# Kernel tuning notes

Measured on AMD Instinct MI355X. Metric: run time of the kernel, lower is better.

## Reference

```python
import jax, jax.numpy as jnp
from jax import lax
import numpy as np

B, C, FH, FW, H, V, L = 256, 512, 8, 16, 512, 64, 24


def setup_inputs() -> dict:
    key = jax.random.key(0)
    ks = jax.random.split(key, 32)
    s = 0.05
    n = lambda k, shp: jax.random.normal(k, shp, dtype=jnp.float32) * s
    return {
        "encoder_ftrs": jax.random.normal(ks[0], (B, C, FH, FW), dtype=jnp.float32),
        "sequences": jax.random.randint(ks[1], (B, L), 0, V),
        "test": 0,
        "embed_w": n(ks[2], (V, H)),
        "init_state": n(ks[3], (2, 1, H)),
        "attn_W_w": n(ks[4], (H, C)), "attn_W_b": jnp.zeros((H,), jnp.float32),
        "attn_U_w": n(ks[5], (H, H)), "attn_U_b": jnp.zeros((H,), jnp.float32),
        "attn_v_w": n(ks[6], (1, H)), "attn_v_b": jnp.zeros((1,), jnp.float32),
        "fc_w": n(ks[7], (H, C + H)), "fc_b": jnp.zeros((H,), jnp.float32),
        "cls_w": n(ks[8], (V, H)), "cls_b": jnp.zeros((V,), jnp.float32),
        "gru0_wih": n(ks[9], (3 * H, 2 * H)), "gru0_whh": n(ks[10], (3 * H, H)),
        "gru0_bih": jnp.zeros((3 * H,), jnp.float32), "gru0_bhh": jnp.zeros((3 * H,), jnp.float32),
        "gru1_wih": n(ks[11], (3 * H, H)), "gru1_whh": n(ks[12], (3 * H, H)),
        "gru1_bih": jnp.zeros((3 * H,), jnp.float32), "gru1_bhh": jnp.zeros((3 * H,), jnp.float32),
    }


def _gru_cell(x, h, wih, whh, bih, bhh):
    # PyTorch GRUCell: r,z gates then candidate n with r applied on hidden path
    gi = x @ wih.T + bih
    gh = h @ whh.T + bhh
    i_r, i_z, i_n = jnp.split(gi, 3, axis=-1)
    h_r, h_z, h_n = jnp.split(gh, 3, axis=-1)
    r = jax.nn.sigmoid(i_r + h_r)
    z = jax.nn.sigmoid(i_z + h_z)
    nact = jnp.tanh(i_n + r * h_n)
    return (1.0 - z) * nact + z * h


def reference(encoder_ftrs, sequences, test, embed_w, init_state,
              attn_W_w, attn_W_b, attn_U_w, attn_U_b, attn_v_w, attn_v_b,
              fc_w, fc_b, cls_w, cls_b,
              gru0_wih, gru0_whh, gru0_bih, gru0_bhh,
              gru1_wih, gru1_whh, gru1_bih, gru1_bhh):
    bsz = encoder_ftrs.shape[0]
    # [B, L_sp, C] encoder states
    states = encoder_ftrs.reshape(bsz, C, -1).transpose(0, 2, 1)
    # attn_W(states) is timestep-independent: precompute once (same math)
    Ws = states @ attn_W_w.T + attn_W_b  # [B, L_sp, H]

    def apply_attn(h_top):
        e = jax.nn.relu(Ws + (h_top @ attn_U_w.T + attn_U_b)[:, None, :])
        scores = e @ attn_v_w[0] + attn_v_b[0]          # [B, L_sp]
        a = jax.nn.softmax(scores, axis=-1)
        ctx = jnp.einsum('bl,blc->bc', a, states)        # [B, C]
        return ctx

    def out_proj(ctx, h_top):
        return jax.nn.relu(jnp.concatenate([ctx, h_top], axis=-1) @ fc_w.T + fc_b)

    xs = embed_w[sequences[:, :-1]]                      # [B, T, H]
    h0 = jnp.broadcast_to(init_state, (2, bsz, H))       # repeat over batch
    y0 = out_proj(apply_attn(h0[1]), h0[1])              # time_step == -1 (output dropped)

    def step(carry, x_t):
        h, y = carry
        h_l0 = _gru_cell(jnp.concatenate([y, x_t], axis=-1), h[0],
                         gru0_wih, gru0_whh, gru0_bih, gru0_bhh)
        h_l1 = _gru_cell(h_l0, h[1], gru1_wih, gru1_whh, gru1_bih, gru1_bhh)
        hn = jnp.stack([h_l0, h_l1], axis=0)
        yn = out_proj(apply_attn(h_l1), h_l1)
        return (hn, yn), yn

    _, ys = lax.scan(step, (h0, y0), xs.transpose(1, 0, 2))   # [T, B, H]
    logits = ys.transpose(1, 0, 2) @ cls_w.T + cls_b          # [B, T, V]

    labels = sequences[:, 1:]
    mask = (labels > 0).astype(logits.dtype)
    logp = jax.nn.log_softmax(logits, axis=-1)
    nll = -jnp.take_along_axis(logp, labels[..., None], axis=-1)[..., 0]
    loss = jnp.sum(nll * mask) / jnp.sum(mask)
    return loss
```

## Files before the change

kernel.cpp:

```cpp
#include <hip/hip_runtime.h>
#include <hip/hip_bf16.h>
#include <cstddef>

#define BB 256
#define CC 512
#define SS 128
#define HH 512
#define VV 64
#define LL 24

typedef unsigned short ush;
typedef __attribute__((ext_vector_type(8))) short short8;
typedef __attribute__((ext_vector_type(4))) float f32x4;

__device__ __forceinline__ float wave_sum(float v) {
#pragma unroll
    for (int off = 32; off > 0; off >>= 1) v += __shfl_xor(v, off);
    return v;
}
__device__ __forceinline__ float wave_max(float v) {
#pragma unroll
    for (int off = 32; off > 0; off >>= 1) v = fmaxf(v, __shfl_xor(v, off));
    return v;
}
__device__ __forceinline__ float sigm(float x) { return 1.0f / (1.0f + expf(-x)); }
__device__ __forceinline__ ush f2bf(float f) {
    unsigned u = __float_as_uint(f);
    u += 0x7FFFu + ((u >> 16) & 1u);
    return (ush)(u >> 16);
}
__device__ __forceinline__ float bf2f(ush b) {
    return __uint_as_float(((unsigned)b) << 16);
}
__device__ __forceinline__ unsigned pack2(float a, float b) {
    return (unsigned)f2bf(a) | ((unsigned)f2bf(b) << 16);
}

__global__ __launch_bounds__(256) void init_kernel(const float* __restrict__ init_state,
                                                   float* __restrict__ h0,
                                                   float* __restrict__ h1,
                                                   ush* __restrict__ h0b,
                                                   ush* __restrict__ h1b,
                                                   float* __restrict__ acc) {
    int idx = blockIdx.x * 256 + threadIdx.x;
    if (idx < BB * HH) {
        float a = init_state[idx & (HH - 1)];
        float b = init_state[HH + (idx & (HH - 1))];
        h0[idx] = a; h1[idx] = b;
        h0b[idx] = f2bf(a); h1b[idx] = f2bf(b);
    }
    if (idx < 2) acc[idx] = 0.0f;
}

__global__ __launch_bounds__(256) void conv_kernel(const float* __restrict__ src,
                                                   ush* __restrict__ dst, int n4) {
    int i = blockIdx.x * 256 + threadIdx.x;
    if (i < n4) {
        float4 v = ((const float4*)src)[i];
        uint2 o;
        o.x = pack2(v.x, v.y);
        o.y = pack2(v.z, v.w);
        ((uint2*)dst)[i] = o;
    }
}

__global__ __launch_bounds__(128) void gather_kernel(const float* __restrict__ embed_w,
                                                     const int* __restrict__ seq,
                                                     ush* __restrict__ xall) {
    int item = blockIdx.x;
    int t = item >> 8, m = item & 255;
    int row = seq[m * LL + t];
    float4 v = ((const float4*)(embed_w + (size_t)row * HH))[threadIdx.x];
    uint2 o;
    o.x = pack2(v.x, v.y);
    o.y = pack2(v.z, v.w);
    ((uint2*)(xall + (size_t)item * HH))[threadIdx.x] = o;
}

__global__ __launch_bounds__(256) void enc_conv(const float* __restrict__ enc,
                                                ush* __restrict__ enc_t) {
    int b = blockIdx.x, cg = blockIdx.y;
    int c0 = cg * 128;
    __shared__ ush tile[128][130];
    const float* src = enc + ((size_t)b * 512 + c0) * 128;
#pragma unroll
    for (int i = 0; i < 16; i++) {
        int lin = i * 256 + threadIdx.x;
        int cl = lin >> 5, s4 = lin & 31;
        float4 v = ((const float4*)(src + (size_t)cl * 128))[s4];
        ush b0 = f2bf(v.x), b1 = f2bf(v.y), b2 = f2bf(v.z), b3 = f2bf(v.w);
        tile[s4 * 4 + 0][cl] = b0;
        tile[s4 * 4 + 1][cl] = b1;
        tile[s4 * 4 + 2][cl] = b2;
        tile[s4 * 4 + 3][cl] = b3;
    }
    __syncthreads();
#pragma unroll
    for (int i = 0; i < 16; i++) {
        int lin = i * 256 + threadIdx.x;
        int sl = lin >> 5, c4 = lin & 31;
        ush a0 = tile[sl][c4 * 4 + 0], a1 = tile[sl][c4 * 4 + 1];
        ush a2 = tile[sl][c4 * 4 + 2], a3 = tile[sl][c4 * 4 + 3];
        uint2 o;
        o.x = (unsigned)a0 | ((unsigned)a1 << 16);
        o.y = (unsigned)a2 | ((unsigned)a3 << 16);
        ((uint2*)(enc_t + ((size_t)b * 128 + sl) * 512 + c0))[c4] = o;
    }
}

__global__ __launch_bounds__(256) void ws_v2(const ush* __restrict__ enc_t,
                                             const ush* __restrict__ Wb,
                                             const float* __restrict__ bias,
                                             ush* __restrict__ Ws_bf) {
    int tid = threadIdx.x;
    int wave = tid >> 6, lane = tid & 63;
    int quad = lane >> 4, l16 = lane & 15;
    int m0 = blockIdx.x * 128 + wave * 32;
    int n0 = blockIdx.y * 128;
    const ush* ap = enc_t + (size_t)(m0 + l16) * 512 + quad * 8;
    const ush* bp = Wb + (size_t)(n0 + l16) * 512 + quad * 8;
    f32x4 acc[2][8];
#pragma unroll
    for (int f = 0; f < 2; f++)
#pragma unroll
        for (int s = 0; s < 8; s++) acc[f][s] = (f32x4){0.f, 0.f, 0.f, 0.f};
    short8 ac[2], bc[8], an[2], bn[8];
    ac[0] = *(const short8*)(ap);
    ac[1] = *(const short8*)(ap + (size_t)16 * 512);
#pragma unroll
    for (int s = 0; s < 8; s++) bc[s] = *(const short8*)(bp + (size_t)s * 16 * 512);
#pragma unroll
    for (int ks = 0; ks < 16; ks++) {
        if (ks < 15) {
            int k = (ks + 1) * 32;
            an[0] = *(const short8*)(ap + k);
            an[1] = *(const short8*)(ap + (size_t)16 * 512 + k);
#pragma unroll
            for (int s = 0; s < 8; s++)
                bn[s] = *(const short8*)(bp + (size_t)s * 16 * 512 + k);
        }
#pragma unroll
        for (int f = 0; f < 2; f++)
#pragma unroll
            for (int s = 0; s < 8; s++)
                acc[f][s] = __builtin_amdgcn_mfma_f32_16x16x32_bf16(ac[f], bc[s], acc[f][s], 0, 0, 0);
        if (ks < 15) {
            ac[0] = an[0]; ac[1] = an[1];
#pragma unroll
            for (int s = 0; s < 8; s++) bc[s] = bn[s];
        }
    }
#pragma unroll
    for (int s = 0; s < 8; s++) {
        int n = n0 + s * 16 + l16;
        float bs = bias[n];
#pragma unroll
        for (int f = 0; f < 2; f++)
#pragma unroll
            for (int r = 0; r < 4; r++) {
                int m = m0 + f * 16 + quad * 4 + r;
                Ws_bf[(size_t)m * HH + n] = f2bf(acc[f][s][r] + bs);
            }
    }
}

template <int NSTEP>
__device__ __forceinline__ void segk(const ush* __restrict__ ap,
                                     const ush* __restrict__ bp,
                                     size_t wofs, f32x4& a0, f32x4& a1) {
    short8 as[4], bs0[4], bs1[4];
    constexpr int PRE = NSTEP < 4 ? NSTEP : 4;
#pragma unroll
    for (int i = 0; i < PRE; i++) {
        as[i]  = *(const short8*)(ap + 32 * i);
        bs0[i] = *(const short8*)(bp + 32 * i);
        bs1[i] = *(const short8*)(bp + wofs + 32 * i);
    }
#pragma unroll
    for (int i = 0; i < NSTEP; i++) {
        const int sl = i & 3;
        a0 = __builtin_amdgcn_mfma_f32_16x16x32_bf16(as[sl], bs0[sl], a0, 0, 0, 0);
        a1 = __builtin_amdgcn_mfma_f32_16x16x32_bf16(as[sl], bs1[sl], a1, 0, 0, 0);
        if (i + 4 < NSTEP) {
            as[sl]  = *(const short8*)(ap + 32 * (i + 4));
            bs0[sl] = *(const short8*)(bp + 32 * (i + 4));
            bs1[sl] = *(const short8*)(bp + wofs + 32 * (i + 4));
        }
    }
}

struct GruArgs {
    const ush* xs[8][2];
    const ush* wb[8][2];
    int wst[8][2];
    int nks[8][2];
    int slot[8][2];
    int zmask;
};

__global__ __launch_bounds__(512) void gru_fused(GruArgs A,
                                                 const float* __restrict__ h_prev,
                                                 const float* __restrict__ bih,
                                                 const float* __restrict__ bhh,
                                                 float* __restrict__ h_out,
                                                 ush* __restrict__ h_out_bf) {
    int tid = threadIdx.x;
    int wave = __builtin_amdgcn_readfirstlane(tid >> 6);
    int lane = tid & 63, quad = lane >> 4, l16 = lane & 15;
    int m0 = blockIdx.x * 16, n0 = blockIdx.y * 32;
    __shared__ float gbuf[10][16][32];
    if (A.zmask) {
        int mi = tid >> 5, ni = tid & 31;
#pragma unroll
        for (int s = 0; s < 10; s++)
            if ((A.zmask >> s) & 1) gbuf[s][mi][ni] = 0.0f;
    }
    for (int e = 0; e < 2; e++) {
        int nks = A.nks[wave][e];
        if (nks == 0) continue;
        f32x4 a0 = (f32x4){0.f, 0.f, 0.f, 0.f};
        f32x4 a1 = (f32x4){0.f, 0.f, 0.f, 0.f};
        int wst = A.wst[wave][e];
        const ush* ap = A.xs[wave][e] + (size_t)(m0 + l16) * 512 + quad * 8;
        const ush* bp = A.wb[wave][e] + (size_t)(n0 + l16) * wst + quad * 8;
        size_t wofs = (size_t)16 * wst;
        if (nks == 16) segk<16>(ap, bp, wofs, a0, a1);
        else           segk<8>(ap, bp, wofs, a0, a1);
        int sl = A.slot[wave][e];
#pragma unroll
        for (int r = 0; r < 4; r++) {
            gbuf[sl][quad * 4 + r][l16]      = a0[r];
            gbuf[sl][quad * 4 + r][16 + l16] = a1[r];
        }
    }
    __syncthreads();
    {
        int mi = tid >> 5, ni = tid & 31;
        int n = n0 + ni;
        size_t off = (size_t)(m0 + mi) * HH + n;
        float r  = sigm(gbuf[0][mi][ni] + gbuf[1][mi][ni] + gbuf[2][mi][ni] +
                        bih[n] + bhh[n]);
        float zf = sigm(gbuf[3][mi][ni] + gbuf[4][mi][ni] + gbuf[5][mi][ni] +
                        bih[512 + n] + bhh[512 + n]);
        float na = tanhf(gbuf[6][mi][ni] + gbuf[7][mi][ni] + bih[1024 + n] +
                         r * (gbuf[8][mi][ni] + gbuf[9][mi][ni] + bhh[1024 + n]));
        float hp = h_prev[off];
        float ho = (1.0f - zf) * na + zf * hp;
        h_out[off] = ho;
        h_out_bf[off] = f2bf(ho);
    }
}

__global__ __launch_bounds__(512) void fc_fused(const ush* __restrict__ ctx,
                                                const ush* __restrict__ h,
                                                const ush* __restrict__ wFc,
                                                const float* __restrict__ bias,
                                                ush* __restrict__ y,
                                                ush* __restrict__ ys) {
    int tid = threadIdx.x;
    int wave = __builtin_amdgcn_readfirstlane(tid >> 6);
    int lane = tid & 63, quad = lane >> 4, l16 = lane & 15;
    int m0 = blockIdx.x * 16, n0 = blockIdx.y * 32;
    const ush* X = (wave < 4) ? ctx : h;
    int q = wave & 3;
    f32x4 a0 = (f32x4){0.f, 0.f, 0.f, 0.f};
    f32x4 a1 = (f32x4){0.f, 0.f, 0.f, 0.f};
    const ush* ap = X + (size_t)(m0 + l16) * 512 + q * 128 + quad * 8;
    const ush* bp = wFc + (size_t)(n0 + l16) * 1024 + (wave >= 4 ? 512 : 0) + q * 128 + quad * 8;
    segk<4>(ap, bp, (size_t)16 * 1024, a0, a1);
    __shared__ float gbuf[8][16][32];
#pragma unroll
    for (int r = 0; r < 4; r++) {
        gbuf[wave][quad * 4 + r][l16]      = a0[r];
        gbuf[wave][quad * 4 + r][16 + l16] = a1[r];
    }
    __syncthreads();
    {
        int mi = tid >> 5, ni = tid & 31;
        int n = n0 + ni;
        float v = bias[n];
#pragma unroll
        for (int w = 0; w < 8; w++) v += gbuf[w][mi][ni];
        v = fmaxf(v, 0.0f);
        ush bb = f2bf(v);
        size_t off = (size_t)(m0 + mi) * HH + n;
        y[off] = bb;
        if (ys) ys[off] = bb;
    }
}

__global__ __launch_bounds__(512) void u_fused(const ush* __restrict__ h,
                                               const ush* __restrict__ wU,
                                               const float* __restrict__ Ub,
                                               float* __restrict__ Uo) {
    int tid = threadIdx.x;
    int wave = __builtin_amdgcn_readfirstlane(tid >> 6);
    int lane = tid & 63, quad = lane >> 4, l16 = lane & 15;
    int m0 = blockIdx.x * 16, n0 = blockIdx.y * 32;
    f32x4 a0 = (f32x4){0.f, 0.f, 0.f, 0.f};
    f32x4 a1 = (f32x4){0.f, 0.f, 0.f, 0.f};
    const ush* ap = h + (size_t)(m0 + l16) * 512 + wave * 64 + quad * 8;
    const ush* bp = wU + (size_t)(n0 + l16) * 512 + wave * 64 + quad * 8;
    segk<2>(ap, bp, (size_t)16 * 512, a0, a1);
    __shared__ float gbuf[8][16][32];
#pragma unroll
    for (int r = 0; r < 4; r++) {
        gbuf[wave][quad * 4 + r][l16]      = a0[r];
        gbuf[wave][quad * 4 + r][16 + l16] = a1[r];
    }
    __syncthreads();
    {
        int mi = tid >> 5, ni = tid & 31;
        int n = n0 + ni;
        float v = Ub[n];
#pragma unroll
        for (int w = 0; w < 8; w++) v += gbuf[w][mi][ni];
        Uo[(size_t)(m0 + mi) * HH + n] = v;
    }
}

__global__ __launch_bounds__(512) void attn3(const float* __restrict__ u,
                                             const float* __restrict__ vw,
                                             const ush* __restrict__ Ws_bf,
                                             const ush* __restrict__ enc_t,
                                             ush* __restrict__ ctx_bf) {
    int b = blockIdx.x;
    int tid = threadIdx.x;
    int wave = tid >> 6, lane = tid & 63;
    int hi = lane >> 4, li = lane & 15;
    __shared__ float a[SS];
    __shared__ float part[8][512];

    float ur[4][8], vr[4][8];
#pragma unroll
    for (int p = 0; p < 4; p++) {
        const float* up = u + (size_t)b * HH + p * 128 + li * 8;
        const float* vp = vw + p * 128 + li * 8;
        float4 u0 = *(const float4*)(up);
        float4 u1 = *(const float4*)(up + 4);
        float4 v0 = *(const float4*)(vp);
        float4 v1 = *(const float4*)(vp + 4);
        ur[p][0] = u0.x; ur[p][1] = u0.y; ur[p][2] = u0.z; ur[p][3] = u0.w;
        ur[p][4] = u1.x; ur[p][5] = u1.y; ur[p][6] = u1.z; ur[p][7] = u1.w;
        vr[p][0] = v0.x; vr[p][1] = v0.y; vr[p][2] = v0.z; vr[p][3] = v0.w;
        vr[p][4] = v1.x; vr[p][5] = v1.y; vr[p][6] = v1.z; vr[p][7] = v1.w;
    }
    const ush* wsb = Ws_bf + (size_t)b * SS * HH;
#pragma unroll
    for (int pass = 0; pass < 4; pass++) {
        int s = pass * 32 + wave * 4 + hi;
        float acc = 0.0f;
#pragma unroll
        for (int p = 0; p < 4; p++) {
            short8 rv = *(const short8*)(wsb + (size_t)s * HH + p * 128 + li * 8);
#pragma unroll
            for (int j = 0; j < 8; j++) {
                float e = bf2f((ush)rv[j]) + ur[p][j];
                acc += fmaxf(e, 0.0f) * vr[p][j];
            }
        }
#pragma unroll
        for (int off = 1; off < 16; off <<= 1) acc += __shfl_xor(acc, off);
        if (li == 0) a[s] = acc;
    }
    __syncthreads();
    if (wave == 0) {
        float s0v = a[lane], s1v = a[lane + 64];
        float m = wave_max(fmaxf(s0v, s1v));
        float e0 = expf(s0v - m), e1 = expf(s1v - m);
        float ssum = wave_sum(e0 + e1);
        float inv = 1.0f / ssum;
        a[lane] = e0 * inv;
        a[lane + 64] = e1 * inv;
    }
    __syncthreads();
    float c8[8];
#pragma unroll
    for (int j = 0; j < 8; j++) c8[j] = 0.0f;
    const ush* ebt = enc_t + (size_t)b * SS * 512;
#pragma unroll
    for (int i = 0; i < 16; i++) {
        int s = wave * 16 + i;
        float as = a[s];
        short8 ev = *(const short8*)(ebt + (size_t)s * 512 + lane * 8);
#pragma unroll
        for (int j = 0; j < 8; j++) c8[j] += as * bf2f((ush)ev[j]);
    }
    *(float4*)(&part[wave][lane * 8])     = (float4){c8[0], c8[1], c8[2], c8[3]};
    *(float4*)(&part[wave][lane * 8 + 4]) = (float4){c8[4], c8[5], c8[6], c8[7]};
    __syncthreads();
    {
        float sum = 0.0f;
#pragma unroll
        for (int w = 0; w < 8; w++) sum += part[w][tid];
        ctx_bf[(size_t)b * CC + tid] = f2bf(sum);
    }
}

__global__ __launch_bounds__(256) void cls_fused(const ush* __restrict__ ys,
                                                 const ush* __restrict__ wCls,
                                                 const float* __restrict__ cls_b,
                                                 const int* __restrict__ seq,
                                                 float* __restrict__ acc) {
    int tid = threadIdx.x;
    int wave = tid >> 6, lane = tid & 63;
    int quad = lane >> 4, l16 = lane & 15;
    int m0 = blockIdx.x * 16;
    f32x4 a4[4];
#pragma unroll
    for (int s = 0; s < 4; s++) a4[s] = (f32x4){0.f, 0.f, 0.f, 0.f};
    const ush* ap = ys + (size_t)(m0 + l16) * 512 + wave * 128 + quad * 8;
    const ush* bp = wCls + (size_t)l16 * 512 + wave * 128 + quad * 8;
#pragma unroll
    for (int ks = 0; ks < 4; ks++) {
        short8 av = *(const short8*)(ap + ks * 32);
#pragma unroll
        for (int s = 0; s < 4; s++) {
            short8 bv = *(const short8*)(bp + (size_t)s * 16 * 512 + ks * 32);
            a4[s] = __builtin_amdgcn_mfma_f32_16x16x32_bf16(av, bv, a4[s], 0, 0, 0);
        }
    }
    __shared__ float gbuf[4][16][64];
    __shared__ float red[8];
#pragma unroll
    for (int s = 0; s < 4; s++)
#pragma unroll
        for (int r = 0; r < 4; r++)
            gbuf[wave][quad * 4 + r][s * 16 + l16] = a4[s][r];
    __syncthreads();
    float lsum = 0.0f, lcnt = 0.0f;
#pragma unroll
    for (int ii = 0; ii < 4; ii++) {
        int mi = wave * 4 + ii;
        int item = m0 + mi;
        int t = item >> 8, b = item & 255;
        float v = gbuf[0][mi][lane] + gbuf[1][mi][lane] + gbuf[2][mi][lane] +
                  gbuf[3][mi][lane] + cls_b[lane];
        float mx = wave_max(v);
        float e = expf(v - mx);
        float ssum = wave_sum(e);
        int label = seq[b * LL + t + 1];
        float vl = __shfl(v, label);
        if (label > 0) {
            lsum += -(vl - mx - logf(ssum));
            lcnt += 1.0f;
        }
    }
    if (lane == 0) { red[wave] = lsum; red[4 + wave] = lcnt; }
    __syncthreads();
    if (tid == 0) {
        atomicAdd(&acc[0], red[0] + red[1] + red[2] + red[3]);
        atomicAdd(&acc[1], red[4] + red[5] + red[6] + red[7]);
    }
}

__global__ void final_kernel(const float* __restrict__ acc, float* __restrict__ out) {
    if (threadIdx.x == 0) out[0] = acc[0] / acc[1];
}

extern "C" void kernel_launch(void* const* d_in, const int* in_sizes, int n_in,
                              void* d_out, int out_size, void* d_ws, size_t ws_size,
                              hipStream_t stream) {
    const float* enc        = (const float*)d_in[0];
    const int*   seq        = (const int*)d_in[1];
    const float* embed_w    = (const float*)d_in[3];
    const float* init_state = (const float*)d_in[4];
    const float* attn_W_w   = (const float*)d_in[5];
    const float* attn_W_b   = (const float*)d_in[6];
    const float* attn_U_w   = (const float*)d_in[7];
    const float* attn_U_b   = (const float*)d_in[8];
    const float* attn_v_w   = (const float*)d_in[9];
    const float* fc_w       = (const float*)d_in[11];
    const float* fc_b       = (const float*)d_in[12];
    const float* cls_w      = (const float*)d_in[13];
    const float* cls_b      = (const float*)d_in[14];
    const float* g0_wih     = (const float*)d_in[15];
    const float* g0_whh     = (const float*)d_in[16];
    const float* g0_bih     = (const float*)d_in[17];
    const float* g0_bhh     = (const float*)d_in[18];
    const float* g1_wih     = (const float*)d_in[19];
    const float* g1_whh     = (const float*)d_in[20];
    const float* g1_bih     = (const float*)d_in[21];
    const float* g1_bhh     = (const float*)d_in[22];
    float* out = (float*)d_out;

    float* ws = (float*)d_ws;
    size_t o = 0;
    ush* Ws_bf   = (ush*)(ws + o); o += (size_t)BB * SS * HH / 2;
    ush* enc_t   = (ush*)(ws + o); o += (size_t)BB * CC * SS / 2;
    ush* ys_bf   = (ush*)(ws + o); o += (size_t)(LL - 1) * BB * HH / 2;
    ush* xall_bf = (ush*)(ws + o); o += (size_t)(LL - 1) * BB * HH / 2;
    ush* wWb  = (ush*)(ws + o); o += 262144 / 2;
    ush* wU   = (ush*)(ws + o); o += 262144 / 2;
    ush* wFc  = (ush*)(ws + o); o += 524288 / 2;
    ush* wCls = (ush*)(ws + o); o += 32768 / 2;
    ush* wG0i = (ush*)(ws + o); o += 1572864 / 2;
    ush* wG0h = (ush*)(ws + o); o += 786432 / 2;
    ush* wG1i = (ush*)(ws + o); o += 786432 / 2;
    ush* wG1h = (ush*)(ws + o); o += 786432 / 2;
    float* Uo   = ws + o; o += (size_t)BB * HH;
    float* h0a  = ws + o; o += (size_t)BB * HH;
    float* h0b  = ws + o; o += (size_t)BB * HH;
    float* h1a  = ws + o; o += (size_t)BB * HH;
    float* h1b  = ws + o; o += (size_t)BB * HH;
    float* acc  = ws + o; o += 256;
    ush* h0a_bf = (ush*)(ws + o); o += (size_t)BB * HH / 2;
    ush* h0b_bf = (ush*)(ws + o); o += (size_t)BB * HH / 2;
    ush* h1a_bf = (ush*)(ws + o); o += (size_t)BB * HH / 2;
    ush* h1b_bf = (ush*)(ws + o); o += (size_t)BB * HH / 2;
    ush* y_bf   = (ush*)(ws + o); o += (size_t)BB * HH / 2;
    ush* ctx_bf = (ush*)(ws + o); o += (size_t)BB * CC / 2;

    init_kernel<<<512, 256, 0, stream>>>(init_state, h0a, h1a, h0a_bf, h1a_bf, acc);
    conv_kernel<<<256, 256, 0, stream>>>(attn_W_w, wWb, 65536);
    conv_kernel<<<256, 256, 0, stream>>>(attn_U_w, wU, 65536);
    conv_kernel<<<512, 256, 0, stream>>>(fc_w, wFc, 131072);
    conv_kernel<<<32, 256, 0, stream>>>(cls_w, wCls, 8192);
    conv_kernel<<<1536, 256, 0, stream>>>(g0_wih, wG0i, 393216);
    conv_kernel<<<768, 256, 0, stream>>>(g0_whh, wG0h, 196608);
    conv_kernel<<<768, 256, 0, stream>>>(g1_wih, wG1i, 196608);
    conv_kernel<<<768, 256, 0, stream>>>(g1_whh, wG1h, 196608);
    enc_conv<<<dim3(256, 4), 256, 0, stream>>>(enc, enc_t);
    gather_kernel<<<(LL - 1) * BB, 128, 0, stream>>>(embed_w, seq, xall_bf);
    ws_v2<<<dim3(256, 4), 256, 0, stream>>>(enc_t, wWb, attn_W_b, Ws_bf);

    auto setw = [](GruArgs& a, int w, int e, const ush* xs, const ush* wb,
                   int wst, int nks, int slot) {
        a.xs[w][e] = xs; a.wb[w][e] = wb; a.wst[w][e] = wst;
        a.nks[w][e] = nks; a.slot[w][e] = slot;
    };
    auto gru0_args = [&](const ush* y, const ush* x, const ush* h0) {
        GruArgs a{};
        setw(a, 0, 0, y,        wG0i,                             1024, 16, 0);
        setw(a, 1, 0, x,        wG0i + 512,                       1024, 16, 1);
        setw(a, 2, 0, h0,       wG0h,                              512, 16, 2);
        setw(a, 3, 0, y,        wG0i + (size_t)512 * 1024,        1024, 16, 3);
        setw(a, 4, 0, x,        wG0i + (size_t)512 * 1024 + 512,  1024, 16, 4);
        setw(a, 5, 0, h0,       wG0h + (size_t)512 * 512,          512, 16, 5);
        setw(a, 6, 0, y,        wG0i + (size_t)1024 * 1024,       1024, 16, 6);
        setw(a, 7, 0, x,        wG0i + (size_t)1024 * 1024 + 512, 1024, 16, 7);
        setw(a, 6, 1, h0,       wG0h + (size_t)1024 * 512,         512,  8, 8);
        setw(a, 7, 1, h0 + 256, wG0h + (size_t)1024 * 512 + 256,   512,  8, 9);
        a.zmask = 0;
        return a;
    };
    auto gru1_args = [&](const ush* hl0, const ush* h1) {
        GruArgs a{};
        setw(a, 0, 0, hl0,       wG1i,                             512, 16, 0);
        setw(a, 1, 0, h1,        wG1h,                             512, 16, 1);
        setw(a, 2, 0, hl0,       wG1i + (size_t)512 * 512,         512, 16, 3);
        setw(a, 3, 0, h1,        wG1h + (size_t)512 * 512,         512, 16, 4);
        setw(a, 4, 0, hl0,       wG1i + (size_t)1024 * 512,        512,  8, 6);
        setw(a, 5, 0, hl0 + 256, wG1i + (size_t)1024 * 512 + 256,  512,  8, 7);
        setw(a, 6, 0, h1,        wG1h + (size_t)1024 * 512,        512,  8, 8);
        setw(a, 7, 0, h1 + 256,  wG1h + (size_t)1024 * 512 + 256,  512,  8, 9);
        a.zmask = (1 << 2) | (1 << 5);
        return a;
    };

    u_fused<<<dim3(16, 16), 512, 0, stream>>>(h1a_bf, wU, attn_U_b, Uo);
    attn3<<<BB, 512, 0, stream>>>(Uo, attn_v_w, Ws_bf, enc_t, ctx_bf);
    fc_fused<<<dim3(16, 16), 512, 0, stream>>>(ctx_bf, h1a_bf, wFc, fc_b, y_bf, nullptr);

    float* h0_in = h0a; float* h0_out = h0b;
    float* h1_in = h1a; float* h1_out = h1b;
    ush* h0_in_bf = h0a_bf; ush* h0_out_bf = h0b_bf;
    ush* h1_in_bf = h1a_bf; ush* h1_out_bf = h1b_bf;
    for (int t = 0; t < LL - 1; t++) {
        gru_fused<<<dim3(16, 16), 512, 0, stream>>>(
            gru0_args(y_bf, xall_bf + (size_t)t * BB * HH, h0_in_bf),
            h0_in, g0_bih, g0_bhh, h0_out, h0_out_bf);
        gru_fused<<<dim3(16, 16), 512, 0, stream>>>(
            gru1_args(h0_out_bf, h1_in_bf),
            h1_in, g1_bih, g1_bhh, h1_out, h1_out_bf);
        u_fused<<<dim3(16, 16), 512, 0, stream>>>(h1_out_bf, wU, attn_U_b, Uo);
        attn3<<<BB, 512, 0, stream>>>(Uo, attn_v_w, Ws_bf, enc_t, ctx_bf);
        fc_fused<<<dim3(16, 16), 512, 0, stream>>>(ctx_bf, h1_out_bf, wFc, fc_b,
                                                   y_bf, ys_bf + (size_t)t * BB * HH);
        float* tmp;
        tmp = h0_in; h0_in = h0_out; h0_out = tmp;
        tmp = h1_in; h1_in = h1_out; h1_out = tmp;
        ush* tb;
        tb = h0_in_bf; h0_in_bf = h0_out_bf; h0_out_bf = tb;
        tb = h1_in_bf; h1_in_bf = h1_out_bf; h1_out_bf = tb;
    }

    cls_fused<<<368, 256, 0, stream>>>(ys_bf, wCls, cls_b, seq, acc);
    final_kernel<<<1, 1, 0, stream>>>(acc, out);
}
```

Baseline: 1.395 ms.

## Fuse U-projection, attention and fc into one per-batch kernel; retile GRU and prep

```diff
diff --git a/kernel.cpp b/kernel.cpp
--- a/kernel.cpp
+++ b/kernel.cpp
@@ -32,6 +32,8 @@
 __device__ __forceinline__ float bf2f(ush b) {
     return __uint_as_float(((unsigned)b) << 16);
 }
+__device__ __forceinline__ float bfl(unsigned u) { return __uint_as_float(u << 16); }
+__device__ __forceinline__ float bfh(unsigned u) { return __uint_as_float(u & 0xFFFF0000u); }
 __device__ __forceinline__ unsigned pack2(float a, float b) {
     return (unsigned)f2bf(a) | ((unsigned)f2bf(b) << 16);
 }
@@ -52,15 +54,50 @@
     if (idx < 2) acc[idx] = 0.0f;
 }
 
-__global__ __launch_bounds__(256) void conv_kernel(const float* __restrict__ src,
-                                                   ush* __restrict__ dst, int n4) {
-    int i = blockIdx.x * 256 + threadIdx.x;
-    if (i < n4) {
-        float4 v = ((const float4*)src)[i];
+struct CvArgs {
+    const float* src[6];
+    ush* dst[6];
+    int end[6];
+};
+__global__ __launch_bounds__(256) void conv_multi(CvArgs A) {
+    int blk = blockIdx.x;
+    int s = 0;
+    while (s < 5 && blk >= A.end[s]) s++;
+    int base = s ? A.end[s - 1] : 0;
+    int i = (blk - base) * 256 + threadIdx.x;
+    float4 v = ((const float4*)A.src[s])[i];
+    uint2 o;
+    o.x = pack2(v.x, v.y);
+    o.y = pack2(v.z, v.w);
+    ((uint2*)A.dst[s])[i] = o;
+}
+
+__global__ __launch_bounds__(256) void tp_conv(const float* __restrict__ src,
+                                               uint2* __restrict__ dst, int K) {
+    int n0 = blockIdx.x * 64, k0 = blockIdx.y * 64;
+    __shared__ ush til[64][68];
+    int tid = threadIdx.x;
+#pragma unroll
+    for (int i = 0; i < 4; i++) {
+        int idx = i * 256 + tid;
+        int r = idx >> 4, c4 = idx & 15;
+        float4 v = ((const float4*)(src + (size_t)(n0 + r) * K + k0))[c4];
+        til[r][c4 * 4 + 0] = f2bf(v.x);
+        til[r][c4 * 4 + 1] = f2bf(v.y);
+        til[r][c4 * 4 + 2] = f2bf(v.z);
+        til[r][c4 * 4 + 3] = f2bf(v.w);
+    }
+    __syncthreads();
+#pragma unroll
+    for (int i = 0; i < 4; i++) {
+        int idx = i * 256 + tid;
+        int k4l = idx >> 6, nl = idx & 63;
+        ush t0 = til[nl][k4l * 4 + 0], t1 = til[nl][k4l * 4 + 1];
+        ush t2 = til[nl][k4l * 4 + 2], t3 = til[nl][k4l * 4 + 3];
         uint2 o;
-        o.x = pack2(v.x, v.y);
-        o.y = pack2(v.z, v.w);
-        ((uint2*)dst)[i] = o;
+        o.x = (unsigned)t0 | ((unsigned)t1 << 16);
+        o.y = (unsigned)t2 | ((unsigned)t3 << 16);
+        dst[(size_t)(k0 / 4 + k4l) * 512 + n0 + nl] = o;
     }
 }
 
@@ -88,11 +125,10 @@
         int lin = i * 256 + threadIdx.x;
         int cl = lin >> 5, s4 = lin & 31;
         float4 v = ((const float4*)(src + (size_t)cl * 128))[s4];
-        ush b0 = f2bf(v.x), b1 = f2bf(v.y), b2 = f2bf(v.z), b3 = f2bf(v.w);
-        tile[s4 * 4 + 0][cl] = b0;
-        tile[s4 * 4 + 1][cl] = b1;
-        tile[s4 * 4 + 2][cl] = b2;
-        tile[s4 * 4 + 3][cl] = b3;
+        tile[s4 * 4 + 0][cl] = f2bf(v.x);
+        tile[s4 * 4 + 1][cl] = f2bf(v.y);
+        tile[s4 * 4 + 2][cl] = f2bf(v.z);
+        tile[s4 * 4 + 3][cl] = f2bf(v.w);
     }
     __syncthreads();
 #pragma unroll
@@ -108,54 +144,56 @@
     }
 }
 
-__global__ __launch_bounds__(256) void ws_v2(const ush* __restrict__ enc_t,
+__global__ __launch_bounds__(512) void ws_v3(const ush* __restrict__ enc_t,
                                              const ush* __restrict__ Wb,
                                              const float* __restrict__ bias,
                                              ush* __restrict__ Ws_bf) {
     int tid = threadIdx.x;
     int wave = tid >> 6, lane = tid & 63;
     int quad = lane >> 4, l16 = lane & 15;
-    int m0 = blockIdx.x * 128 + wave * 32;
-    int n0 = blockIdx.y * 128;
+    int m0 = blockIdx.x * 128 + (wave & 1) * 64;
+    int n0 = blockIdx.y * 128 + (wave >> 1) * 32;
     const ush* ap = enc_t + (size_t)(m0 + l16) * 512 + quad * 8;
     const ush* bp = Wb + (size_t)(n0 + l16) * 512 + quad * 8;
-    f32x4 acc[2][8];
-#pragma unroll
-    for (int f = 0; f < 2; f++)
-#pragma unroll
-        for (int s = 0; s < 8; s++) acc[f][s] = (f32x4){0.f, 0.f, 0.f, 0.f};
-    short8 ac[2], bc[8], an[2], bn[8];
-    ac[0] = *(const short8*)(ap);
-    ac[1] = *(const short8*)(ap + (size_t)16 * 512);
-#pragma unroll
-    for (int s = 0; s < 8; s++) bc[s] = *(const short8*)(bp + (size_t)s * 16 * 512);
+    f32x4 acc[4][2];
+#pragma unroll
+    for (int f = 0; f < 4; f++)
+#pragma unroll
+        for (int s = 0; s < 2; s++) acc[f][s] = (f32x4){0.f, 0.f, 0.f, 0.f};
+    short8 ac[4], bc[2], an[4], bn[2];
+#pragma unroll
+    for (int f = 0; f < 4; f++) ac[f] = *(const short8*)(ap + (size_t)f * 16 * 512);
+#pragma unroll
+    for (int s = 0; s < 2; s++) bc[s] = *(const short8*)(bp + (size_t)s * 16 * 512);
 #pragma unroll
     for (int ks = 0; ks < 16; ks++) {
         if (ks < 15) {
             int k = (ks + 1) * 32;
-            an[0] = *(const short8*)(ap + k);
-            an[1] = *(const short8*)(ap + (size_t)16 * 512 + k);
-#pragma unroll
-            for (int s = 0; s < 8; s++)
+#pragma unroll
+            for (int f = 0; f < 4; f++)
+                an[f] = *(const short8*)(ap + (size_t)f * 16 * 512 + k);
+#pragma unroll
+            for (int s = 0; s < 2; s++)
                 bn[s] = *(const short8*)(bp + (size_t)s * 16 * 512 + k);
         }
 #pragma unroll
-        for (int f = 0; f < 2; f++)
-#pragma unroll
-            for (int s = 0; s < 8; s++)
+        for (int f = 0; f < 4; f++)
+#pragma unroll
+            for (int s = 0; s < 2; s++)
                 acc[f][s] = __builtin_amdgcn_mfma_f32_16x16x32_bf16(ac[f], bc[s], acc[f][s], 0, 0, 0);
         if (ks < 15) {
-            ac[0] = an[0]; ac[1] = an[1];
-#pragma unroll
-            for (int s = 0; s < 8; s++) bc[s] = bn[s];
-        }
-    }
-#pragma unroll
-    for (int s = 0; s < 8; s++) {
+#pragma unroll
+            for (int f = 0; f < 4; f++) ac[f] = an[f];
+#pragma unroll
+            for (int s = 0; s < 2; s++) bc[s] = bn[s];
+        }
+    }
+#pragma unroll
+    for (int s = 0; s < 2; s++) {
         int n = n0 + s * 16 + l16;
         float bs = bias[n];
 #pragma unroll
-        for (int f = 0; f < 2; f++)
+        for (int f = 0; f < 4; f++)
 #pragma unroll
             for (int r = 0; r < 4; r++) {
                 int m = m0 + f * 16 + quad * 4 + r;
@@ -165,38 +203,28 @@
 }
 
 template <int NSTEP>
-__device__ __forceinline__ void segk(const ush* __restrict__ ap,
-                                     const ush* __restrict__ bp,
-                                     size_t wofs, f32x4& a0, f32x4& a1) {
-    short8 as[4], bs0[4], bs1[4];
+__device__ __forceinline__ void segk1(const ush* __restrict__ ap,
+                                      const ush* __restrict__ bp, f32x4& a0) {
+    short8 as[4], bs[4];
     constexpr int PRE = NSTEP < 4 ? NSTEP : 4;
 #pragma unroll
     for (int i = 0; i < PRE; i++) {
-        as[i]  = *(const short8*)(ap + 32 * i);
-        bs0[i] = *(const short8*)(bp + 32 * i);
-        bs1[i] = *(const short8*)(bp + wofs + 32 * i);
+        as[i] = *(const short8*)(ap + 32 * i);
+        bs[i] = *(const short8*)(bp + 32 * i);
     }
 #pragma unroll
     for (int i = 0; i < NSTEP; i++) {
         const int sl = i & 3;
-        a0 = __builtin_amdgcn_mfma_f32_16x16x32_bf16(as[sl], bs0[sl], a0, 0, 0, 0);
-        a1 = __builtin_amdgcn_mfma_f32_16x16x32_bf16(as[sl], bs1[sl], a1, 0, 0, 0);
+        a0 = __builtin_amdgcn_mfma_f32_16x16x32_bf16(as[sl], bs[sl], a0, 0, 0, 0);
         if (i + 4 < NSTEP) {
-            as[sl]  = *(const short8*)(ap + 32 * (i + 4));
-            bs0[sl] = *(const short8*)(bp + 32 * (i + 4));
-            bs1[sl] = *(const short8*)(bp + wofs + 32 * (i + 4));
-        }
-    }
-}
-
-struct GruArgs {
-    const ush* xs[8][2];
-    const ush* wb[8][2];
-    int wst[8][2];
-    int nks[8][2];
-    int slot[8][2];
-    int zmask;
-};
+            as[sl] = *(const short8*)(ap + 32 * (i + 4));
+            bs[sl] = *(const short8*)(bp + 32 * (i + 4));
+        }
+    }
+}
+
+struct GruEnt { const ush* x; const ush* w; int wst; int nks; int slot; };
+struct GruArgs { GruEnt e[8][2]; int zmask; };
 
 __global__ __launch_bounds__(512) void gru_fused(GruArgs A,
                                                  const float* __restrict__ h_prev,
@@ -207,43 +235,41 @@
     int tid = threadIdx.x;
     int wave = __builtin_amdgcn_readfirstlane(tid >> 6);
     int lane = tid & 63, quad = lane >> 4, l16 = lane & 15;
-    int m0 = blockIdx.x * 16, n0 = blockIdx.y * 32;
-    __shared__ float gbuf[10][16][32];
-    if (A.zmask) {
-        int mi = tid >> 5, ni = tid & 31;
-#pragma unroll
-        for (int s = 0; s < 10; s++)
+    int m0 = blockIdx.x * 16, n0 = blockIdx.y * 16;
+    __shared__ float gbuf[14][16][16];
+    if (tid < 256 && A.zmask) {
+        int mi = tid >> 4, ni = tid & 15;
+#pragma unroll
+        for (int s = 0; s < 14; s++)
             if ((A.zmask >> s) & 1) gbuf[s][mi][ni] = 0.0f;
     }
+#pragma unroll
     for (int e = 0; e < 2; e++) {
-        int nks = A.nks[wave][e];
-        if (nks == 0) continue;
+        GruEnt ent = A.e[wave][e];
+        if (ent.nks == 0) continue;
         f32x4 a0 = (f32x4){0.f, 0.f, 0.f, 0.f};
-        f32x4 a1 = (f32x4){0.f, 0.f, 0.f, 0.f};
-        int wst = A.wst[wave][e];
-        const ush* ap = A.xs[wave][e] + (size_t)(m0 + l16) * 512 + quad * 8;
-        const ush* bp = A.wb[wave][e] + (size_t)(n0 + l16) * wst + quad * 8;
-        size_t wofs = (size_t)16 * wst;
-        if (nks == 16) segk<16>(ap, bp, wofs, a0, a1);
-        else           segk<8>(ap, bp, wofs, a0, a1);
-        int sl = A.slot[wave][e];
-#pragma unroll
-        for (int r = 0; r < 4; r++) {
-            gbuf[sl][quad * 4 + r][l16]      = a0[r];
-            gbuf[sl][quad * 4 + r][16 + l16] = a1[r];
-        }
-    }
-    __syncthreads();
-    {
-        int mi = tid >> 5, ni = tid & 31;
+        const ush* ap = ent.x + (size_t)(m0 + l16) * 512 + quad * 8;
+        const ush* bp = ent.w + (size_t)(n0 + l16) * ent.wst + quad * 8;
+        if (ent.nks == 16)      segk1<16>(ap, bp, a0);
+        else if (ent.nks == 12) segk1<12>(ap, bp, a0);
+        else if (ent.nks == 8)  segk1<8>(ap, bp, a0);
+        else                    segk1<4>(ap, bp, a0);
+#pragma unroll
+        for (int r = 0; r < 4; r++)
+            gbuf[ent.slot][quad * 4 + r][l16] = a0[r];
+    }
+    __syncthreads();
+    if (tid < 256) {
+        int mi = tid >> 4, ni = tid & 15;
         int n = n0 + ni;
         size_t off = (size_t)(m0 + mi) * HH + n;
-        float r  = sigm(gbuf[0][mi][ni] + gbuf[1][mi][ni] + gbuf[2][mi][ni] +
-                        bih[n] + bhh[n]);
-        float zf = sigm(gbuf[3][mi][ni] + gbuf[4][mi][ni] + gbuf[5][mi][ni] +
-                        bih[512 + n] + bhh[512 + n]);
-        float na = tanhf(gbuf[6][mi][ni] + gbuf[7][mi][ni] + bih[1024 + n] +
-                         r * (gbuf[8][mi][ni] + gbuf[9][mi][ni] + bhh[1024 + n]));
+        float rr = sigm(gbuf[0][mi][ni] + gbuf[1][mi][ni] + gbuf[2][mi][ni] +
+                        gbuf[3][mi][ni] + bih[n] + bhh[n]);
+        float zf = sigm(gbuf[4][mi][ni] + gbuf[5][mi][ni] + gbuf[6][mi][ni] +
+                        gbuf[7][mi][ni] + bih[512 + n] + bhh[512 + n]);
+        float na = tanhf(gbuf[8][mi][ni] + gbuf[9][mi][ni] + bih[1024 + n] +
+                         rr * (gbuf[10][mi][ni] + gbuf[11][mi][ni] +
+                               gbuf[12][mi][ni] + gbuf[13][mi][ni] + bhh[1024 + n]));
         float hp = h_prev[off];
         float ho = (1.0f - zf) * na + zf * hp;
         h_out[off] = ho;
@@ -251,93 +277,49 @@
     }
 }
 
-__global__ __launch_bounds__(512) void fc_fused(const ush* __restrict__ ctx,
-                                                const ush* __restrict__ h,
-                                                const ush* __restrict__ wFc,
-                                                const float* __restrict__ bias,
-                                                ush* __restrict__ y,
-                                                ush* __restrict__ ys) {
-    int tid = threadIdx.x;
-    int wave = __builtin_amdgcn_readfirstlane(tid >> 6);
-    int lane = tid & 63, quad = lane >> 4, l16 = lane & 15;
-    int m0 = blockIdx.x * 16, n0 = blockIdx.y * 32;
-    const ush* X = (wave < 4) ? ctx : h;
-    int q = wave & 3;
-    f32x4 a0 = (f32x4){0.f, 0.f, 0.f, 0.f};
-    f32x4 a1 = (f32x4){0.f, 0.f, 0.f, 0.f};
-    const ush* ap = X + (size_t)(m0 + l16) * 512 + q * 128 + quad * 8;
-    const ush* bp = wFc + (size_t)(n0 + l16) * 1024 + (wave >= 4 ? 512 : 0) + q * 128 + quad * 8;
-    segk<4>(ap, bp, (size_t)16 * 1024, a0, a1);
-    __shared__ float gbuf[8][16][32];
-#pragma unroll
-    for (int r = 0; r < 4; r++) {
-        gbuf[wave][quad * 4 + r][l16]      = a0[r];
-        gbuf[wave][quad * 4 + r][16 + l16] = a1[r];
-    }
-    __syncthreads();
-    {
-        int mi = tid >> 5, ni = tid & 31;
-        int n = n0 + ni;
-        float v = bias[n];
-#pragma unroll
-        for (int w = 0; w < 8; w++) v += gbuf[w][mi][ni];
-        v = fmaxf(v, 0.0f);
-        ush bb = f2bf(v);
-        size_t off = (size_t)(m0 + mi) * HH + n;
-        y[off] = bb;
-        if (ys) ys[off] = bb;
-    }
-}
-
-__global__ __launch_bounds__(512) void u_fused(const ush* __restrict__ h,
-                                               const ush* __restrict__ wU,
-                                               const float* __restrict__ Ub,
-                                               float* __restrict__ Uo) {
-    int tid = threadIdx.x;
-    int wave = __builtin_amdgcn_readfirstlane(tid >> 6);
-    int lane = tid & 63, quad = lane >> 4, l16 = lane & 15;
-    int m0 = blockIdx.x * 16, n0 = blockIdx.y * 32;
-    f32x4 a0 = (f32x4){0.f, 0.f, 0.f, 0.f};
-    f32x4 a1 = (f32x4){0.f, 0.f, 0.f, 0.f};
-    const ush* ap = h + (size_t)(m0 + l16) * 512 + wave * 64 + quad * 8;
-    const ush* bp = wU + (size_t)(n0 + l16) * 512 + wave * 64 + quad * 8;
-    segk<2>(ap, bp, (size_t)16 * 512, a0, a1);
-    __shared__ float gbuf[8][16][32];
-#pragma unroll
-    for (int r = 0; r < 4; r++) {
-        gbuf[wave][quad * 4 + r][l16]      = a0[r];
-        gbuf[wave][quad * 4 + r][16 + l16] = a1[r];
-    }
-    __syncthreads();
-    {
-        int mi = tid >> 5, ni = tid & 31;
-        int n = n0 + ni;
-        float v = Ub[n];
-#pragma unroll
-        for (int w = 0; w < 8; w++) v += gbuf[w][mi][ni];
-        Uo[(size_t)(m0 + mi) * HH + n] = v;
-    }
-}
-
-__global__ __launch_bounds__(512) void attn3(const float* __restrict__ u,
-                                             const float* __restrict__ vw,
-                                             const ush* __restrict__ Ws_bf,
-                                             const ush* __restrict__ enc_t,
-                                             ush* __restrict__ ctx_bf) {
+__global__ __launch_bounds__(512) void uaf(const float* __restrict__ h1f,
+                                           const uint2* __restrict__ wUt,
+                                           const float* __restrict__ Ub,
+                                           const float* __restrict__ vw,
+                                           const ush* __restrict__ Ws_bf,
+                                           const ush* __restrict__ enc_t,
+                                           const uint2* __restrict__ wFcT,
+                                           const float* __restrict__ fc_b,
+                                           ush* __restrict__ y_bf,
+                                           ush* __restrict__ ys_bf) {
     int b = blockIdx.x;
     int tid = threadIdx.x;
     int wave = tid >> 6, lane = tid & 63;
     int hi = lane >> 4, li = lane & 15;
+    __shared__ float h1s[512];
+    __shared__ float u_lds[512];
+    __shared__ float ctx[512];
     __shared__ float a[SS];
     __shared__ float part[8][512];
 
+    h1s[tid] = h1f[(size_t)b * HH + tid];
+    __syncthreads();
+
+    {
+        float acc = Ub[tid];
+        const uint2* wp = wUt + tid;
+#pragma unroll 8
+        for (int kq = 0; kq < 128; kq++) {
+            uint2 pr = wp[(size_t)kq * 512];
+            float x0 = h1s[kq * 4 + 0], x1 = h1s[kq * 4 + 1];
+            float x2 = h1s[kq * 4 + 2], x3 = h1s[kq * 4 + 3];
+            acc += bfl(pr.x) * x0 + bfh(pr.x) * x1 + bfl(pr.y) * x2 + bfh(pr.y) * x3;
+        }
+        u_lds[tid] = acc;
+    }
+    __syncthreads();
+
     float ur[4][8], vr[4][8];
 #pragma unroll
     for (int p = 0; p < 4; p++) {
-        const float* up = u + (size_t)b * HH + p * 128 + li * 8;
+        float4 u0 = *(const float4*)(&u_lds[p * 128 + li * 8]);
+        float4 u1 = *(const float4*)(&u_lds[p * 128 + li * 8 + 4]);
         const float* vp = vw + p * 128 + li * 8;
-        float4 u0 = *(const float4*)(up);
-        float4 u1 = *(const float4*)(up + 4);
         float4 v0 = *(const float4*)(vp);
         float4 v1 = *(const float4*)(vp + 4);
         ur[p][0] = u0.x; ur[p][1] = u0.y; ur[p][2] = u0.z; ur[p][3] = u0.w;
@@ -364,6 +346,7 @@
         if (li == 0) a[s] = acc;
     }
     __syncthreads();
+
     if (wave == 0) {
         float s0v = a[lane], s1v = a[lane + 64];
         float m = wave_max(fmaxf(s0v, s1v));
@@ -374,26 +357,54 @@
         a[lane + 64] = e1 * inv;
     }
     __syncthreads();
-    float c8[8];
-#pragma unroll
-    for (int j = 0; j < 8; j++) c8[j] = 0.0f;
-    const ush* ebt = enc_t + (size_t)b * SS * 512;
-#pragma unroll
-    for (int i = 0; i < 16; i++) {
-        int s = wave * 16 + i;
-        float as = a[s];
-        short8 ev = *(const short8*)(ebt + (size_t)s * 512 + lane * 8);
-#pragma unroll
-        for (int j = 0; j < 8; j++) c8[j] += as * bf2f((ush)ev[j]);
-    }
-    *(float4*)(&part[wave][lane * 8])     = (float4){c8[0], c8[1], c8[2], c8[3]};
-    *(float4*)(&part[wave][lane * 8 + 4]) = (float4){c8[4], c8[5], c8[6], c8[7]};
+
+    {
+        float c8[8];
+#pragma unroll
+        for (int j = 0; j < 8; j++) c8[j] = 0.0f;
+        const ush* ebt = enc_t + (size_t)b * SS * 512;
+#pragma unroll
+        for (int i = 0; i < 16; i++) {
+            int s = wave * 16 + i;
+            float as = a[s];
+            short8 ev = *(const short8*)(ebt + (size_t)s * 512 + lane * 8);
+#pragma unroll
+            for (int j = 0; j < 8; j++) c8[j] += as * bf2f((ush)ev[j]);
+        }
+        *(float4*)(&part[wave][lane * 8])     = (float4){c8[0], c8[1], c8[2], c8[3]};
+        *(float4*)(&part[wave][lane * 8 + 4]) = (float4){c8[4], c8[5], c8[6], c8[7]};
+    }
     __syncthreads();
     {
         float sum = 0.0f;
 #pragma unroll
         for (int w = 0; w < 8; w++) sum += part[w][tid];
-        ctx_bf[(size_t)b * CC + tid] = f2bf(sum);
+        ctx[tid] = sum;
+    }
+    __syncthreads();
+
+    {
+        float acc = fc_b[tid];
+        const uint2* wp = wFcT + tid;
+#pragma unroll 8
+        for (int kq = 0; kq < 128; kq++) {
+            uint2 pr = wp[(size_t)kq * 512];
+            float x0 = ctx[kq * 4 + 0], x1 = ctx[kq * 4 + 1];
+            float x2 = ctx[kq * 4 + 2], x3 = ctx[kq * 4 + 3];
+            acc += bfl(pr.x) * x0 + bfh(pr.x) * x1 + bfl(pr.y) * x2 + bfh(pr.y) * x3;
+        }
+#pragma unroll 8
+        for (int kq = 128; kq < 256; kq++) {
+            uint2 pr = wp[(size_t)kq * 512];
+            int k = kq * 4 - 512;
+            float x0 = h1s[k + 0], x1 = h1s[k + 1];
+            float x2 = h1s[k + 2], x3 = h1s[k + 3];
+            acc += bfl(pr.x) * x0 + bfh(pr.x) * x1 + bfl(pr.y) * x2 + bfh(pr.y) * x3;
+        }
+        float v = fmaxf(acc, 0.0f);
+        ush bb = f2bf(v);
+        y_bf[(size_t)b * HH + tid] = bb;
+        if (ys_bf) ys_bf[(size_t)b * HH + tid] = bb;
     }
 }
 
@@ -491,14 +502,13 @@
     ush* ys_bf   = (ush*)(ws + o); o += (size_t)(LL - 1) * BB * HH / 2;
     ush* xall_bf = (ush*)(ws + o); o += (size_t)(LL - 1) * BB * HH / 2;
     ush* wWb  = (ush*)(ws + o); o += 262144 / 2;
-    ush* wU   = (ush*)(ws + o); o += 262144 / 2;
-    ush* wFc  = (ush*)(ws + o); o += 524288 / 2;
     ush* wCls = (ush*)(ws + o); o += 32768 / 2;
     ush* wG0i = (ush*)(ws + o); o += 1572864 / 2;
     ush* wG0h = (ush*)(ws + o); o += 786432 / 2;
     ush* wG1i = (ush*)(ws + o); o += 786432 / 2;
     ush* wG1h = (ush*)(ws + o); o += 786432 / 2;
-    float* Uo   = ws + o; o += (size_t)BB * HH;
+    uint2* wUt  = (uint2*)(ws + o); o += 131072;
+    uint2* wFcT = (uint2*)(ws + o); o += 262144;
     float* h0a  = ws + o; o += (size_t)BB * HH;
     float* h0b  = ws + o; o += (size_t)BB * HH;
     float* h1a  = ws + o; o += (size_t)BB * HH;
@@ -509,74 +519,82 @@
     ush* h1a_bf = (ush*)(ws + o); o += (size_t)BB * HH / 2;
     ush* h1b_bf = (ush*)(ws + o); o += (size_t)BB * HH / 2;
     ush* y_bf   = (ush*)(ws + o); o += (size_t)BB * HH / 2;
-    ush* ctx_bf = (ush*)(ws + o); o += (size_t)BB * CC / 2;
 
     init_kernel<<<512, 256, 0, stream>>>(init_state, h0a, h1a, h0a_bf, h1a_bf, acc);
-    conv_kernel<<<256, 256, 0, stream>>>(attn_W_w, wWb, 65536);
-    conv_kernel<<<256, 256, 0, stream>>>(attn_U_w, wU, 65536);
-    conv_kernel<<<512, 256, 0, stream>>>(fc_w, wFc, 131072);
-    conv_kernel<<<32, 256, 0, stream>>>(cls_w, wCls, 8192);
-    conv_kernel<<<1536, 256, 0, stream>>>(g0_wih, wG0i, 393216);
-    conv_kernel<<<768, 256, 0, stream>>>(g0_whh, wG0h, 196608);
-    conv_kernel<<<768, 256, 0, stream>>>(g1_wih, wG1i, 196608);
-    conv_kernel<<<768, 256, 0, stream>>>(g1_whh, wG1h, 196608);
+    {
+        CvArgs cv{};
+        cv.src[0] = attn_W_w; cv.dst[0] = wWb;
+        cv.src[1] = cls_w;    cv.dst[1] = wCls;
+        cv.src[2] = g0_wih;   cv.dst[2] = wG0i;
+        cv.src[3] = g0_whh;   cv.dst[3] = wG0h;
+        cv.src[4] = g1_wih;   cv.dst[4] = wG1i;
+        cv.src[5] = g1_whh;   cv.dst[5] = wG1h;
+        cv.end[0] = 256; cv.end[1] = 288; cv.end[2] = 1824;
+        cv.end[3] = 2592; cv.end[4] = 3360; cv.end[5] = 4128;
+        conv_multi<<<4128, 256, 0, stream>>>(cv);
+    }
+    tp_conv<<<dim3(8, 8), 256, 0, stream>>>(attn_U_w, wUt, 512);
+    tp_conv<<<dim3(8, 16), 256, 0, stream>>>(fc_w, wFcT, 1024);
     enc_conv<<<dim3(256, 4), 256, 0, stream>>>(enc, enc_t);
     gather_kernel<<<(LL - 1) * BB, 128, 0, stream>>>(embed_w, seq, xall_bf);
-    ws_v2<<<dim3(256, 4), 256, 0, stream>>>(enc_t, wWb, attn_W_b, Ws_bf);
-
-    auto setw = [](GruArgs& a, int w, int e, const ush* xs, const ush* wb,
-                   int wst, int nks, int slot) {
-        a.xs[w][e] = xs; a.wb[w][e] = wb; a.wst[w][e] = wst;
-        a.nks[w][e] = nks; a.slot[w][e] = slot;
+    ws_v3<<<dim3(256, 4), 512, 0, stream>>>(enc_t, wWb, attn_W_b, Ws_bf);
+
+    auto E = [](GruArgs& a, int w, int e, const ush* x, const ush* wp, int wst,
+                int nks, int slot) {
+        a.e[w][e].x = x; a.e[w][e].w = wp; a.e[w][e].wst = wst;
+        a.e[w][e].nks = nks; a.e[w][e].slot = slot;
     };
     auto gru0_args = [&](const ush* y, const ush* x, const ush* h0) {
         GruArgs a{};
-        setw(a, 0, 0, y,        wG0i,                             1024, 16, 0);
-        setw(a, 1, 0, x,        wG0i + 512,                       1024, 16, 1);
-        setw(a, 2, 0, h0,       wG0h,                              512, 16, 2);
-        setw(a, 3, 0, y,        wG0i + (size_t)512 * 1024,        1024, 16, 3);
-        setw(a, 4, 0, x,        wG0i + (size_t)512 * 1024 + 512,  1024, 16, 4);
-        setw(a, 5, 0, h0,       wG0h + (size_t)512 * 512,          512, 16, 5);
-        setw(a, 6, 0, y,        wG0i + (size_t)1024 * 1024,       1024, 16, 6);
-        setw(a, 7, 0, x,        wG0i + (size_t)1024 * 1024 + 512, 1024, 16, 7);
-        setw(a, 6, 1, h0,       wG0h + (size_t)1024 * 512,         512,  8, 8);
-        setw(a, 7, 1, h0 + 256, wG0h + (size_t)1024 * 512 + 256,   512,  8, 9);
-        a.zmask = 0;
+        E(a, 0, 0, y,        wG0i,                              1024, 16, 0);
+        E(a, 1, 0, x,        wG0i + 512,                        1024, 16, 1);
+        E(a, 2, 0, h0,       wG0h,                               512, 16, 2);
+        E(a, 3, 0, y,        wG0i + (size_t)512 * 1024,         1024, 16, 4);
+        E(a, 4, 0, x,        wG0i + (size_t)512 * 1024 + 512,   1024, 16, 5);
+        E(a, 5, 0, h0,       wG0h + (size_t)512 * 512,           512, 16, 6);
+        E(a, 6, 0, y,        wG0i + (size_t)1024 * 1024,        1024, 16, 8);
+        E(a, 7, 0, x,        wG0i + (size_t)1024 * 1024 + 512,  1024, 16, 9);
+        E(a, 2, 1, h0,       wG0h + (size_t)1024 * 512,          512,  4, 10);
+        E(a, 3, 1, h0 + 128, wG0h + (size_t)1024 * 512 + 128,    512,  4, 11);
+        E(a, 4, 1, h0 + 256, wG0h + (size_t)1024 * 512 + 256,    512,  4, 12);
+        E(a, 5, 1, h0 + 384, wG0h + (size_t)1024 * 512 + 384,    512,  4, 13);
+        a.zmask = (1 << 3) | (1 << 7);
         return a;
     };
-    auto gru1_args = [&](const ush* hl0, const ush* h1) {
+    auto gru1_args = [&](const ush* hi_, const ush* hh) {
         GruArgs a{};
-        setw(a, 0, 0, hl0,       wG1i,                             512, 16, 0);
-        setw(a, 1, 0, h1,        wG1h,                             512, 16, 1);
-        setw(a, 2, 0, hl0,       wG1i + (size_t)512 * 512,         512, 16, 3);
-        setw(a, 3, 0, h1,        wG1h + (size_t)512 * 512,         512, 16, 4);
-        setw(a, 4, 0, hl0,       wG1i + (size_t)1024 * 512,        512,  8, 6);
-        setw(a, 5, 0, hl0 + 256, wG1i + (size_t)1024 * 512 + 256,  512,  8, 7);
-        setw(a, 6, 0, h1,        wG1h + (size_t)1024 * 512,        512,  8, 8);
-        setw(a, 7, 0, h1 + 256,  wG1h + (size_t)1024 * 512 + 256,  512,  8, 9);
-        a.zmask = (1 << 2) | (1 << 5);
+        E(a, 0, 0, hi_,       wG1i,                             512, 12, 0);
+        E(a, 1, 0, hh,        wG1h,                             512, 12, 2);
+        E(a, 2, 0, hi_,       wG1i + (size_t)512 * 512,         512, 12, 4);
+        E(a, 3, 0, hh,        wG1h + (size_t)512 * 512,         512, 12, 6);
+        E(a, 4, 0, hi_,       wG1i + (size_t)1024 * 512,        512,  8, 8);
+        E(a, 4, 1, hi_ + 384, wG1i + 384,                       512,  4, 1);
+        E(a, 5, 0, hi_ + 256, wG1i + (size_t)1024 * 512 + 256,  512,  8, 9);
+        E(a, 5, 1, hh + 384,  wG1h + 384,                       512,  4, 3);
+        E(a, 6, 0, hh,        wG1h + (size_t)1024 * 512,        512,  8, 10);
+        E(a, 6, 1, hi_ + 384, wG1i + (size_t)512 * 512 + 384,   512,  4, 5);
+        E(a, 7, 0, hh + 256,  wG1h + (size_t)1024 * 512 + 256,  512,  8, 11);
+        E(a, 7, 1, hh + 384,  wG1h + (size_t)512 * 512 + 384,   512,  4, 7);
+        a.zmask = (1 << 12) | (1 << 13);
         return a;
     };
 
-    u_fused<<<dim3(16, 16), 512, 0, stream>>>(h1a_bf, wU, attn_U_b, Uo);
-    attn3<<<BB, 512, 0, stream>>>(Uo, attn_v_w, Ws_bf, enc_t, ctx_bf);
-    fc_fused<<<dim3(16, 16), 512, 0, stream>>>(ctx_bf, h1a_bf, wFc, fc_b, y_bf, nullptr);
+    uaf<<<BB, 512, 0, stream>>>(h1a, wUt, attn_U_b, attn_v_w, Ws_bf, enc_t,
+                                wFcT, fc_b, y_bf, nullptr);
 
     float* h0_in = h0a; float* h0_out = h0b;
     float* h1_in = h1a; float* h1_out = h1b;
     ush* h0_in_bf = h0a_bf; ush* h0_out_bf = h0b_bf;
     ush* h1_in_bf = h1a_bf; ush* h1_out_bf = h1b_bf;
     for (int t = 0; t < LL - 1; t++) {
-        gru_fused<<<dim3(16, 16), 512, 0, stream>>>(
+        gru_fused<<<dim3(16, 32), 512, 0, stream>>>(
             gru0_args(y_bf, xall_bf + (size_t)t * BB * HH, h0_in_bf),
             h0_in, g0_bih, g0_bhh, h0_out, h0_out_bf);
-        gru_fused<<<dim3(16, 16), 512, 0, stream>>>(
+        gru_fused<<<dim3(16, 32), 512, 0, stream>>>(
             gru1_args(h0_out_bf, h1_in_bf),
             h1_in, g1_bih, g1_bhh, h1_out, h1_out_bf);
-        u_fused<<<dim3(16, 16), 512, 0, stream>>>(h1_out_bf, wU, attn_U_b, Uo);
-        attn3<<<BB, 512, 0, stream>>>(Uo, attn_v_w, Ws_bf, enc_t, ctx_bf);
-        fc_fused<<<dim3(16, 16), 512, 0, stream>>>(ctx_bf, h1_out_bf, wFc, fc_b,
-                                                   y_bf, ys_bf + (size_t)t * BB * HH);
+        uaf<<<BB, 512, 0, stream>>>(h1_out, wUt, attn_U_b, attn_v_w, Ws_bf, enc_t,
+                                    wFcT, fc_b, y_bf, ys_bf + (size_t)t * BB * HH);
         float* tmp;
         tmp = h0_in; h0_in = h0_out; h0_out = tmp;
         tmp = h1_in; h1_in = h1_out; h1_out = tmp;
```

New measurement: 1.925 ms. 38.0% more time.
